# Performance work log

Measured on AMD Instinct MI355X. Metric: run time of the kernel, lower is better.

## Reference

```python
import jax, jax.numpy as jnp
import numpy as np
import math

N_HEADS = 16

def _apply_rope(t, cos, sin):
    # t: [b, h, s, hd]; cos/sin: [s, hd//2] (interleaved pairs, llama2.c style)
    b, h, s, hd = t.shape
    tr = t.reshape(b, h, s, hd // 2, 2)
    x_r, x_i = tr[..., 0], tr[..., 1]
    c = cos[None, None, :, :]
    sn = sin[None, None, :, :]
    o_r = x_r * c - x_i * sn
    o_i = x_r * sn + x_i * c
    return jnp.stack([o_r, o_i], axis=-1).reshape(b, h, s, hd)

def setup_inputs() -> dict:
    key = jax.random.key(0)
    ks = jax.random.split(key, 7)
    b, s, d = 4, 2048, 2048
    hd = d // N_HEADS
    x = jax.random.normal(ks[0], (b, s, d), dtype=jnp.float32)
    # RoPE tables: cos/sin of theta * pos, standard 10000 base
    inv_freq = 1.0 / (10000.0 ** (np.arange(0, hd, 2, dtype=np.float32) / hd))
    pos = np.arange(s, dtype=np.float32)
    ang = np.outer(pos, inv_freq)  # [s, hd/2]
    freq_cos = jnp.asarray(np.cos(ang), dtype=jnp.float32)
    freq_sin = jnp.asarray(np.sin(ang), dtype=jnp.float32)
    Wqkv = jax.random.normal(ks[1], (d, 3 * d), dtype=jnp.float32) * (1.0 / math.sqrt(d))
    bqkv = jnp.zeros((3 * d,), dtype=jnp.float32)
    Wout = jax.random.normal(ks[2], (d, d), dtype=jnp.float32) * (1.0 / math.sqrt(d))
    bout = jnp.zeros((d,), dtype=jnp.float32)
    return {"x": x, "freq_cos": freq_cos, "freq_sin": freq_sin,
            "Wqkv": Wqkv, "bqkv": bqkv, "Wout": Wout, "bout": bout}

def reference(x, freq_cos, freq_sin, Wqkv, bqkv, Wout, bout):
    b, s, d = x.shape
    hd = d // N_HEADS
    qkv = x @ Wqkv + bqkv                       # [b, s, 3d]
    q, k, v = jnp.split(qkv, 3, axis=-1)
    def to_heads(t):
        return t.reshape(b, s, N_HEADS, hd).transpose(0, 2, 1, 3)  # [b, h, s, hd]
    q, k, v = to_heads(q), to_heads(k), to_heads(v)
    q = _apply_rope(q, freq_cos, freq_sin)
    k = _apply_rope(k, freq_cos, freq_sin)
    att = jnp.einsum('bhqd,bhkd->bhqk', q, k) / math.sqrt(hd)
    mask = jnp.tril(jnp.ones((s, s), dtype=bool))
    att = jnp.where(mask[None, None, :, :], att, -jnp.inf)
    att = jax.nn.softmax(att, axis=-1)
    y = jnp.einsum('bhqk,bhkd->bhqd', att, v)
    y = y.transpose(0, 2, 1, 3).reshape(b, s, d)
    return y @ Wout + bout
```

## Files before the change

kernel.cpp:

```cpp
#include <hip/hip_runtime.h>

typedef __attribute__((ext_vector_type(4))) float f32x4;
typedef __attribute__((ext_vector_type(8))) short bf16x8;
typedef __attribute__((ext_vector_type(4))) unsigned int uint4v;
typedef __attribute__((ext_vector_type(4))) unsigned short ushort4v;
typedef unsigned short u16;
typedef unsigned int u32;

#define AS1(p) ((const __attribute__((address_space(1))) u32*)(p))
#define AS3(p) ((__attribute__((address_space(3))) u32*)(p))

__device__ __forceinline__ float bf2f(u16 v) {
    u32 u = ((u32)v) << 16;
    return __builtin_bit_cast(float, u);
}
__device__ __forceinline__ u16 f2bf(float f) {
    u32 u = __builtin_bit_cast(u32, f);
    u += 0x7fffu + ((u >> 16) & 1u);
    return (u16)(u >> 16);
}

__global__ __launch_bounds__(256) void k_cvt_bf16(const float* __restrict__ in,
                                                  u16* __restrict__ out, int n8) {
    int t = blockIdx.x * 256 + threadIdx.x;
    if (t >= n8) return;
    const f32x4* p = (const f32x4*)in + (size_t)t * 2;
    f32x4 a = p[0], b = p[1];
    uint4v o;
    o[0] = (u32)f2bf(a[0]) | ((u32)f2bf(a[1]) << 16);
    o[1] = (u32)f2bf(a[2]) | ((u32)f2bf(a[3]) << 16);
    o[2] = (u32)f2bf(b[0]) | ((u32)f2bf(b[1]) << 16);
    o[3] = (u32)f2bf(b[2]) | ((u32)f2bf(b[3]) << 16);
    *((uint4v*)(out + (size_t)t * 8)) = o;
}

__global__ __launch_bounds__(256) void k_transpose_bf16(const float* __restrict__ in,
                                                        u16* __restrict__ out,
                                                        int R, int C) {
    __shared__ float tile[32][33];
    const int bx = blockIdx.x * 32, by = blockIdx.y * 32;
    const int tx = threadIdx.x & 31, ty = threadIdx.x >> 5;
#pragma unroll
    for (int i = 0; i < 32; i += 8)
        tile[ty + i][tx] = in[(size_t)(by + ty + i) * C + bx + tx];
    __syncthreads();
#pragma unroll
    for (int i = 0; i < 32; i += 8)
        out[(size_t)(bx + ty + i) * R + by + tx] = f2bf(tile[tx][ty + i]);
}

template <int OUT_BF16>
__global__ __launch_bounds__(512, 2) void k_gemm256(const u16* __restrict__ A,
                                                    const u16* __restrict__ Bt,
                                                    const float* __restrict__ bias,
                                                    void* __restrict__ Cout,
                                                    int M, int N, int K) {
    __shared__ u16 lds[65536];
    const int tid = threadIdx.x;
    const int wid = tid >> 6, l = tid & 63;
    const int lr = l & 15, lg = l >> 4;
    const int wm = wid >> 2, wn = wid & 3;
    const size_t brow = (size_t)blockIdx.x * 256;
    const size_t bcol = (size_t)blockIdx.y * 256;
    const int KT = K >> 6;

    const u16* gA[4];
    const u16* gB[4];
#pragma unroll
    for (int r = 0; r < 4; ++r) {
        const int P = r * 8 + wid, g = P >> 1, kh = P & 1;
        const size_t off = (size_t)(g * 16 + lr) * K + kh * 32 + lg * 8;
        gA[r] = A + brow * K + off;
        gB[r] = Bt + bcol * K + off;
    }

    f32x4 acc[8][4];
#pragma unroll
    for (int m = 0; m < 8; ++m)
#pragma unroll
        for (int n = 0; n < 4; ++n) acc[m][n] = (f32x4){0.f, 0.f, 0.f, 0.f};

#define STAGE(t)                                                                        \
    do {                                                                                \
        const int b_ = (t) & 1;                                                         \
        const int k0_ = (t) << 6;                                                       \
        u16* dA_ = &lds[b_ * 16384];                                                    \
        u16* dB_ = &lds[32768 + b_ * 16384];                                            \
        __builtin_amdgcn_global_load_lds(AS1(gA[0] + k0_), AS3(dA_ + (0 * 8 + wid) * 512), 16, 0, 0); \
        __builtin_amdgcn_global_load_lds(AS1(gB[0] + k0_), AS3(dB_ + (0 * 8 + wid) * 512), 16, 0, 0); \
        __builtin_amdgcn_global_load_lds(AS1(gA[1] + k0_), AS3(dA_ + (1 * 8 + wid) * 512), 16, 0, 0); \
        __builtin_amdgcn_global_load_lds(AS1(gB[1] + k0_), AS3(dB_ + (1 * 8 + wid) * 512), 16, 0, 0); \
        __builtin_amdgcn_global_load_lds(AS1(gA[2] + k0_), AS3(dA_ + (2 * 8 + wid) * 512), 16, 0, 0); \
        __builtin_amdgcn_global_load_lds(AS1(gB[2] + k0_), AS3(dB_ + (2 * 8 + wid) * 512), 16, 0, 0); \
        __builtin_amdgcn_global_load_lds(AS1(gA[3] + k0_), AS3(dA_ + (3 * 8 + wid) * 512), 16, 0, 0); \
        __builtin_amdgcn_global_load_lds(AS1(gB[3] + k0_), AS3(dB_ + (3 * 8 + wid) * 512), 16, 0, 0); \
    } while (0)

    STAGE(0);
    asm volatile("s_waitcnt vmcnt(0)" ::: "memory");
    __builtin_amdgcn_s_barrier();
    __builtin_amdgcn_sched_barrier(0);

#pragma unroll 1
    for (int t = 0; t < KT; ++t) {
        if (t + 1 < KT) STAGE(t + 1);
        const u16* pa = &lds[(t & 1) * 16384 + wm * 8192 + l * 8];
        const u16* pb = &lds[32768 + (t & 1) * 16384 + wn * 4096 + l * 8];
#pragma unroll
        for (int ks = 0; ks < 2; ++ks) {
            bf16x8 af[8], bfr[4];
#pragma unroll
            for (int m = 0; m < 8; ++m) af[m] = *(const bf16x8*)(pa + (m * 2 + ks) * 512);
#pragma unroll
            for (int n = 0; n < 4; ++n) bfr[n] = *(const bf16x8*)(pb + (n * 2 + ks) * 512);
            __builtin_amdgcn_s_setprio(1);
#pragma unroll
            for (int m = 0; m < 8; ++m)
#pragma unroll
                for (int n = 0; n < 4; ++n)
                    acc[m][n] = __builtin_amdgcn_mfma_f32_16x16x32_bf16(af[m], bfr[n], acc[m][n], 0, 0, 0);
            __builtin_amdgcn_s_setprio(0);
        }
        __builtin_amdgcn_sched_barrier(0);
        asm volatile("s_waitcnt vmcnt(0)" ::: "memory");
        __builtin_amdgcn_s_barrier();
        __builtin_amdgcn_sched_barrier(0);
    }
#undef STAGE

#pragma unroll
    for (int m = 0; m < 8; ++m) {
        const size_t row0 = brow + wm * 128 + m * 16 + lg * 4;
#pragma unroll
        for (int n = 0; n < 4; ++n) {
            const size_t col = bcol + wn * 64 + n * 16 + lr;
            const float bv = bias[col];
#pragma unroll
            for (int r = 0; r < 4; ++r) {
                float v = acc[m][n][r] + bv;
                if (OUT_BF16)
                    ((u16*)Cout)[(row0 + r) * N + col] = f2bf(v);
                else
                    ((float*)Cout)[(row0 + r) * N + col] = v;
            }
        }
    }
}

__global__ __launch_bounds__(256) void k_rope(const u16* __restrict__ qkv,
                                              const float* __restrict__ fcos,
                                              const float* __restrict__ fsin,
                                              u16* __restrict__ qb, u16* __restrict__ kb) {
    const int t = blockIdx.x * 256 + threadIdx.x;
    const int e = t & 7, h = (t >> 3) & 15, r = (t >> 7) & 1, s = (t >> 8) & 2047, b = t >> 19;
    const u16* src = qkv + ((size_t)(b * 2048 + s)) * 6144 + r * 2048 + h * 128 + e * 16;
    uint4v p0 = *(const uint4v*)src;
    uint4v p1 = *(const uint4v*)(src + 8);
    const float* cp = fcos + s * 64 + e * 8;
    const float* sp = fsin + s * 64 + e * 8;
    f32x4 c0 = *(const f32x4*)cp, c1 = *(const f32x4*)(cp + 4);
    f32x4 s0 = *(const f32x4*)sp, s1 = *(const f32x4*)(sp + 4);
    float x[16];
#pragma unroll
    for (int i = 0; i < 4; ++i) {
        x[2 * i]     = bf2f((u16)(p0[i] & 0xffff));
        x[2 * i + 1] = bf2f((u16)(p0[i] >> 16));
        x[8 + 2 * i]     = bf2f((u16)(p1[i] & 0xffff));
        x[8 + 2 * i + 1] = bf2f((u16)(p1[i] >> 16));
    }
    float c[8]  = {c0[0], c0[1], c0[2], c0[3], c1[0], c1[1], c1[2], c1[3]};
    float sn[8] = {s0[0], s0[1], s0[2], s0[3], s1[0], s1[1], s1[2], s1[3]};
    u32 ow[8];
#pragma unroll
    for (int i = 0; i < 8; ++i) {
        float xr = x[2 * i], xi = x[2 * i + 1];
        float orr = xr * c[i] - xi * sn[i];
        float oii = xr * sn[i] + xi * c[i];
        ow[i] = (u32)f2bf(orr) | ((u32)f2bf(oii) << 16);
    }
    u16* dst = (r ? kb : qb) + ((size_t)((b * 16 + h) * 2048 + s)) * 128 + e * 16;
    uint4v q0 = {ow[0], ow[1], ow[2], ow[3]};
    uint4v q1 = {ow[4], ow[5], ow[6], ow[7]};
    *(uint4v*)dst = q0;
    *(uint4v*)(dst + 8) = q1;
}

struct VtRegs { uint4v v0, v1, v2, v3; };

__device__ __forceinline__ void attn_stage_k(const u16* kp, int kbase, u16* dstBase,
                                             int w, int lr, int lg) {
#pragma unroll
    for (int c = 0; c < 4; ++c) {
        const int row = w * 16 + c * 4 + lg;
        const int sslot = lr ^ (4 * (c & 1) + lg);
        const u16* gsrc = kp + (size_t)(kbase + row) * 128 + sslot * 8;
        __builtin_amdgcn_global_load_lds(AS1(gsrc), AS3(dstBase + (w * 16 + c * 4) * 128), 16, 0, 0);
    }
}

__device__ __forceinline__ VtRegs attn_load_v(const u16* vp, int kbase, int tid) {
    const int rg = tid >> 4, cg = tid & 15;
    const u16* gv = vp + (size_t)(kbase + rg * 4) * 6144 + cg * 8;
    VtRegs r;
    r.v0 = *(const uint4v*)gv;
    r.v1 = *(const uint4v*)(gv + 6144);
    r.v2 = *(const uint4v*)(gv + 2 * 6144);
    r.v3 = *(const uint4v*)(gv + 3 * 6144);
    return r;
}

__device__ __forceinline__ void attn_write_v(u16 (*Vt)[64], const VtRegs& r, int tid) {
    const int rg = tid >> 4, cg = tid & 15;
    const u16* u0 = (const u16*)&r.v0;
    const u16* u1 = (const u16*)&r.v1;
    const u16* u2 = (const u16*)&r.v2;
    const u16* u3 = (const u16*)&r.v3;
    const int sb = rg >> 1, hf = (rg & 1) * 4;
#pragma unroll
    for (int cc = 0; cc < 8; ++cc) {
        const int row = cg * 8 + cc;
        const int col = ((sb ^ ((cg ^ cc) & 7)) << 3) + hf;
        ushort4v pk = {u0[cc], u1[cc], u2[cc], u3[cc]};
        *(ushort4v*)&Vt[row][col] = pk;
    }
}

__device__ __forceinline__ void attn_qtile(int qt, const u16* qp, const u16* kp,
                                           const u16* vp, u16* yp,
                                           u16 (*Ks)[64][128], u16 (*Vt)[64],
                                           u16 (*Psw)[72],
                                           int w, int lr, int lg, int tid) {
    const int qw = qt * 128 + w * 32;
    const int l = tid & 63;

    bf16x8 qf[2][4];
#pragma unroll
    for (int i = 0; i < 2; ++i)
#pragma unroll
        for (int ks = 0; ks < 4; ++ks)
            qf[i][ks] = *(const bf16x8*)(qp + (size_t)(qw + i * 16 + lr) * 128 + ks * 32 + lg * 8);

    f32x4 acc[2][8];
#pragma unroll
    for (int i = 0; i < 2; ++i)
#pragma unroll
        for (int j = 0; j < 8; ++j) acc[i][j] = (f32x4){0.f, 0.f, 0.f, 0.f};
    float mrow[2] = {-1e30f, -1e30f}, lrow[2] = {0.f, 0.f};

    const float scale = 0.08838834764831845f;
    const int nkt = 2 * qt + 2;

    VtRegs vr = attn_load_v(vp, 0, tid);
    attn_stage_k(kp, 0, &Ks[0][0][0], w, lr, lg);
    attn_write_v(Vt, vr, tid);
    __syncthreads();

    int cur = 0;
    for (int kt = 0; kt < nkt; ++kt) {
        const int kbase = kt * 64;
        const bool pf = (kt + 1 < nkt);
        if (pf) {
            vr = attn_load_v(vp, kbase + 64, tid);
            attn_stage_k(kp, kbase + 64, &Ks[cur ^ 1][0][0], w, lr, lg);
        }

        if (kbase <= qw + 31) {
            f32x4 st[2][4];
#pragma unroll
            for (int i = 0; i < 2; ++i)
#pragma unroll
                for (int j = 0; j < 4; ++j) st[i][j] = (f32x4){0.f, 0.f, 0.f, 0.f};
#pragma unroll
            for (int nt = 0; nt < 4; ++nt) {
#pragma unroll
                for (int ks = 0; ks < 4; ++ks) {
                    const int slot = (ks * 4 + lg) ^ (lr & 7);
                    bf16x8 kf = *(const bf16x8*)&Ks[cur][nt * 16 + lr][slot * 8];
#pragma unroll
                    for (int mt = 0; mt < 2; ++mt)
                        st[mt][nt] = __builtin_amdgcn_mfma_f32_16x16x32_bf16(kf, qf[mt][ks], st[mt][nt], 0, 0, 0);
                }
            }
            const bool pm = (kbase + 63 > qw);
#pragma unroll
            for (int mt = 0; mt < 2; ++mt)
#pragma unroll
                for (int nt = 0; nt < 4; ++nt)
#pragma unroll
                    for (int r = 0; r < 4; ++r) {
                        float v = st[mt][nt][r] * scale;
                        if (pm) {
                            const int qi = qw + mt * 16 + lr;
                            const int ki = kbase + nt * 16 + lg * 4 + r;
                            if (ki > qi) v = -1e30f;
                        }
                        st[mt][nt][r] = v;
                    }
            float rm[2], fac[2];
#pragma unroll
            for (int mt = 0; mt < 2; ++mt) {
                float m0 = st[mt][0][0];
#pragma unroll
                for (int nt = 0; nt < 4; ++nt)
#pragma unroll
                    for (int r = 0; r < 4; ++r) m0 = fmaxf(m0, st[mt][nt][r]);
                m0 = fmaxf(m0, __shfl_xor(m0, 16));
                m0 = fmaxf(m0, __shfl_xor(m0, 32));
                rm[mt] = m0;
                const float mn = fmaxf(mrow[mt], m0);
                fac[mt] = __expf(mrow[mt] - mn);
                mrow[mt] = mn;
                lrow[mt] *= fac[mt];
            }
            float facr[2][4];
#pragma unroll
            for (int mt = 0; mt < 2; ++mt)
#pragma unroll
                for (int r = 0; r < 4; ++r)
                    facr[mt][r] = __shfl(fac[mt], (l & 48) | (lg * 4 + r));
#pragma unroll
            for (int mt = 0; mt < 2; ++mt)
#pragma unroll
                for (int nt = 0; nt < 8; ++nt)
#pragma unroll
                    for (int r = 0; r < 4; ++r) acc[mt][nt][r] *= facr[mt][r];
#pragma unroll
            for (int mt = 0; mt < 2; ++mt) {
                float rs = 0.f;
#pragma unroll
                for (int nt = 0; nt < 4; ++nt)
#pragma unroll
                    for (int r = 0; r < 4; ++r) {
                        const float p = __expf(st[mt][nt][r] - mrow[mt]);
                        st[mt][nt][r] = p;
                        rs += p;
                    }
                rs += __shfl_xor(rs, 16);
                rs += __shfl_xor(rs, 32);
                lrow[mt] += rs;
            }
#pragma unroll
            for (int mt = 0; mt < 2; ++mt)
#pragma unroll
                for (int nt = 0; nt < 4; ++nt) {
                    const u32 p01 = (u32)f2bf(st[mt][nt][0]) | ((u32)f2bf(st[mt][nt][1]) << 16);
                    const u32 p23 = (u32)f2bf(st[mt][nt][2]) | ((u32)f2bf(st[mt][nt][3]) << 16);
                    u16* dst = &Psw[mt * 16 + lr][nt * 16 + lg * 4];
                    *(u32*)dst = p01;
                    *(u32*)(dst + 2) = p23;
                }
#pragma unroll
            for (int k2 = 0; k2 < 2; ++k2) {
                bf16x8 pa[2];
                pa[0] = *(const bf16x8*)&Psw[lr][k2 * 32 + lg * 8];
                pa[1] = *(const bf16x8*)&Psw[16 + lr][k2 * 32 + lg * 8];
#pragma unroll
                for (int nt = 0; nt < 8; ++nt) {
                    const int f = ((nt * 2 + (lr >> 3)) ^ lr) & 7;
                    const int slot = (k2 * 4 + lg) ^ f;
                    bf16x8 vb = *(const bf16x8*)&Vt[nt * 16 + lr][slot * 8];
#pragma unroll
                    for (int mt = 0; mt < 2; ++mt)
                        acc[mt][nt] = __builtin_amdgcn_mfma_f32_16x16x32_bf16(pa[mt], vb, acc[mt][nt], 0, 0, 0);
                }
            }
        }

        __builtin_amdgcn_s_barrier();
        __builtin_amdgcn_sched_barrier(0);
        if (pf) {
            asm volatile("s_waitcnt vmcnt(4)" ::: "memory");
            attn_write_v(Vt, vr, tid);
            asm volatile("s_waitcnt vmcnt(0) lgkmcnt(0)" ::: "memory");
        } else {
            asm volatile("s_waitcnt vmcnt(0) lgkmcnt(0)" ::: "memory");
        }
        __builtin_amdgcn_s_barrier();
        __builtin_amdgcn_sched_barrier(0);
        cur ^= 1;
    }

#pragma unroll
    for (int mt = 0; mt < 2; ++mt)
#pragma unroll
        for (int r = 0; r < 4; ++r) {
            const float lsum = __shfl(lrow[mt], (l & 48) | (lg * 4 + r));
            const float inv = 1.f / lsum;
            const size_t row = qw + mt * 16 + lg * 4 + r;
#pragma unroll
            for (int nt = 0; nt < 8; ++nt)
                yp[row * 2048 + nt * 16 + lr] = f2bf(acc[mt][nt][r] * inv);
        }
}

__global__ __launch_bounds__(256, 2) void k_attn(const u16* __restrict__ qb,
                                                 const u16* __restrict__ kb,
                                                 const u16* __restrict__ qkv,
                                                 u16* __restrict__ yb) {
    __shared__ u16 Ks[2][64][128];
    __shared__ u16 Vt[128][64];
    __shared__ u16 Ps[4][32][72];

    const int gid = blockIdx.x;
    const int x = gid >> 6;
    const int g = gid & 63;
    const int h = g & 15, b = g >> 4;
    const int tid = threadIdx.x;
    const int w = tid >> 6, l = tid & 63;
    const int lr = l & 15, lg = l >> 4;

    const u16* qp = qb + (size_t)((b * 16 + h) * 2048) * 128;
    const u16* kp = kb + (size_t)((b * 16 + h) * 2048) * 128;
    const u16* vp = qkv + (size_t)(b * 2048) * 6144 + 4096 + h * 128;
    u16* yp = yb + (size_t)(b * 2048) * 2048 + h * 128;

    attn_qtile(x,      qp, kp, vp, yp, Ks, Vt, Ps[w], w, lr, lg, tid);
    attn_qtile(15 - x, qp, kp, vp, yp, Ks, Vt, Ps[w], w, lr, lg, tid);
}

extern "C" void kernel_launch(void* const* d_in, const int* in_sizes, int n_in,
                              void* d_out, int out_size, void* d_ws, size_t ws_size,
                              hipStream_t stream) {
    const float* x    = (const float*)d_in[0];
    const float* fcos = (const float*)d_in[1];
    const float* fsin = (const float*)d_in[2];
    const float* Wqkv = (const float*)d_in[3];
    const float* bqkv = (const float*)d_in[4];
    const float* Wout = (const float*)d_in[5];
    const float* bout = (const float*)d_in[6];
    float* out = (float*)d_out;

    if (ws_size < 234881024u) return;

    char* ws = (char*)d_ws;
    u16* x_bf  = (u16*)(ws);
    u16* wqkvT = (u16*)(ws + 33554432);
    u16* woutT = (u16*)(ws + 58720256);
    u16* qkv   = (u16*)(ws + 67108864);
    u16* qb    = (u16*)(ws + 167772160);
    u16* kb    = (u16*)(ws + 201326592);
    u16* yb    = x_bf;

    k_cvt_bf16<<<8192, 256, 0, stream>>>(x, x_bf, 2097152);
    k_transpose_bf16<<<dim3(192, 64), 256, 0, stream>>>(Wqkv, wqkvT, 2048, 6144);
    k_transpose_bf16<<<dim3(64, 64), 256, 0, stream>>>(Wout, woutT, 2048, 2048);
    k_gemm256<1><<<dim3(32, 24), 512, 0, stream>>>(x_bf, wqkvT, bqkv, qkv, 8192, 6144, 2048);
    k_rope<<<8192, 256, 0, stream>>>(qkv, fcos, fsin, qb, kb);
    k_attn<<<512, 256, 0, stream>>>(qb, kb, qkv, yb);
    k_gemm256<0><<<dim3(32, 8), 512, 0, stream>>>(yb, woutT, bout, out, 8192, 2048, 2048);
}
```

Before: 559.0 us.

## Restructure GEMM main loop into phased quadrant schedule with finer-grained prefetch

Rewrites the 256x256 GEMM K-loop into an unrolled two-tile iteration split into four quadrant phases per tile. Each phase loads a sub-fragment from LDS, issues one slice of the global-to-LDS prefetch for the next tile, and runs its MFMAs between barriers, with partial vmcnt waits in place of full drains. The aim is to interleave memory traffic with compute more evenly and cut register pressure per phase. Launch bounds drop to one block per SM, giving more registers in exchange for less occupancy, and the many extra barriers add synchronisation cost.

New measurement: 519.1 us. 1.08x faster.

```diff
diff --git a/kernel.cpp b/kernel.cpp
--- a/kernel.cpp
+++ b/kernel.cpp
@@ -50,7 +50,7 @@
 }
 
 template <int OUT_BF16>
-__global__ __launch_bounds__(512, 2) void k_gemm256(const u16* __restrict__ A,
+__global__ __launch_bounds__(512, 1) void k_gemm256(const u16* __restrict__ A,
                                                     const u16* __restrict__ Bt,
                                                     const float* __restrict__ bias,
                                                     void* __restrict__ Cout,
@@ -63,16 +63,28 @@
     const size_t brow = (size_t)blockIdx.x * 256;
     const size_t bcol = (size_t)blockIdx.y * 256;
     const int KT = K >> 6;
-
-    const u16* gA[4];
-    const u16* gB[4];
-#pragma unroll
-    for (int r = 0; r < 4; ++r) {
-        const int P = r * 8 + wid, g = P >> 1, kh = P & 1;
-        const size_t off = (size_t)(g * 16 + lr) * K + kh * 32 + lg * 8;
-        gA[r] = A + brow * K + off;
-        gB[r] = Bt + bcol * K + off;
-    }
+    const int NJ = KT >> 1;
+
+    const u16* gArow = A + brow * K;
+    const u16* gBrow = Bt + bcol * K;
+    const size_t laneoff = (size_t)lr * K + lg * 8;
+    const int gA1 = (wid & 3) | ((wid & 4) << 1);
+    const int gA2 = gA1 + 4;
+    const int gB1 = (wid & 1) | ((wid & 6) << 1);
+    const int gB2 = gB1 + 2;
+
+    auto STG = [&](const u16* gbase, int opBase, int g, int tt) {
+        u16* dst = &lds[opBase + ((tt) & 1) * 16384 + g * 1024];
+        const u16* src = gbase + (size_t)g * 16 * K + (size_t)tt * 64 + laneoff;
+        __builtin_amdgcn_global_load_lds(AS1(src), AS3(dst), 16, 0, 0);
+        __builtin_amdgcn_global_load_lds(AS1(src + 32), AS3(dst + 512), 16, 0, 0);
+    };
+    auto LDA_ = [&](int slot, int m, int ks) {
+        return *(const bf16x8*)&lds[slot * 16384 + ((wm * 8 + m) * 2 + ks) * 512 + l * 8];
+    };
+    auto LDB_ = [&](int slot, int n, int ks) {
+        return *(const bf16x8*)&lds[32768 + slot * 16384 + ((wn * 4 + n) * 2 + ks) * 512 + l * 8];
+    };
 
     f32x4 acc[8][4];
 #pragma unroll
@@ -80,53 +92,164 @@
 #pragma unroll
         for (int n = 0; n < 4; ++n) acc[m][n] = (f32x4){0.f, 0.f, 0.f, 0.f};
 
-#define STAGE(t)                                                                        \
-    do {                                                                                \
-        const int b_ = (t) & 1;                                                         \
-        const int k0_ = (t) << 6;                                                       \
-        u16* dA_ = &lds[b_ * 16384];                                                    \
-        u16* dB_ = &lds[32768 + b_ * 16384];                                            \
-        __builtin_amdgcn_global_load_lds(AS1(gA[0] + k0_), AS3(dA_ + (0 * 8 + wid) * 512), 16, 0, 0); \
-        __builtin_amdgcn_global_load_lds(AS1(gB[0] + k0_), AS3(dB_ + (0 * 8 + wid) * 512), 16, 0, 0); \
-        __builtin_amdgcn_global_load_lds(AS1(gA[1] + k0_), AS3(dA_ + (1 * 8 + wid) * 512), 16, 0, 0); \
-        __builtin_amdgcn_global_load_lds(AS1(gB[1] + k0_), AS3(dB_ + (1 * 8 + wid) * 512), 16, 0, 0); \
-        __builtin_amdgcn_global_load_lds(AS1(gA[2] + k0_), AS3(dA_ + (2 * 8 + wid) * 512), 16, 0, 0); \
-        __builtin_amdgcn_global_load_lds(AS1(gB[2] + k0_), AS3(dB_ + (2 * 8 + wid) * 512), 16, 0, 0); \
-        __builtin_amdgcn_global_load_lds(AS1(gA[3] + k0_), AS3(dA_ + (3 * 8 + wid) * 512), 16, 0, 0); \
-        __builtin_amdgcn_global_load_lds(AS1(gB[3] + k0_), AS3(dB_ + (3 * 8 + wid) * 512), 16, 0, 0); \
-    } while (0)
-
-    STAGE(0);
-    asm volatile("s_waitcnt vmcnt(0)" ::: "memory");
+    STG(gArow, 0, gA1, 0); STG(gBrow, 32768, gB1, 0);
+    STG(gArow, 0, gA2, 0); STG(gBrow, 32768, gB2, 0);
+    STG(gArow, 0, gA1, 1); STG(gBrow, 32768, gB1, 1);
+    STG(gArow, 0, gA2, 1);
+    asm volatile("s_waitcnt vmcnt(6)" ::: "memory");
     __builtin_amdgcn_s_barrier();
-    __builtin_amdgcn_sched_barrier(0);
+
+#define OPEN_PHASE()                                              \
+    __builtin_amdgcn_s_barrier();                                 \
+    asm volatile("s_waitcnt lgkmcnt(0)" ::: "memory");            \
+    __builtin_amdgcn_sched_barrier(0);                            \
+    __builtin_amdgcn_s_setprio(1);
+#define CLOSE_PHASE()                                             \
+    __builtin_amdgcn_s_setprio(0);                                \
+    __builtin_amdgcn_sched_barrier(0);                            \
+    __builtin_amdgcn_s_barrier();
 
 #pragma unroll 1
-    for (int t = 0; t < KT; ++t) {
-        if (t + 1 < KT) STAGE(t + 1);
-        const u16* pa = &lds[(t & 1) * 16384 + wm * 8192 + l * 8];
-        const u16* pb = &lds[32768 + (t & 1) * 16384 + wn * 4096 + l * 8];
-#pragma unroll
-        for (int ks = 0; ks < 2; ++ks) {
-            bf16x8 af[8], bfr[4];
-#pragma unroll
-            for (int m = 0; m < 8; ++m) af[m] = *(const bf16x8*)(pa + (m * 2 + ks) * 512);
-#pragma unroll
-            for (int n = 0; n < 4; ++n) bfr[n] = *(const bf16x8*)(pb + (n * 2 + ks) * 512);
-            __builtin_amdgcn_s_setprio(1);
-#pragma unroll
-            for (int m = 0; m < 8; ++m)
-#pragma unroll
-                for (int n = 0; n < 4; ++n)
-                    acc[m][n] = __builtin_amdgcn_mfma_f32_16x16x32_bf16(af[m], bfr[n], acc[m][n], 0, 0, 0);
-            __builtin_amdgcn_s_setprio(0);
-        }
-        __builtin_amdgcn_sched_barrier(0);
-        asm volatile("s_waitcnt vmcnt(0)" ::: "memory");
+    for (int j = 0; j < NJ; ++j) {
+        const int t0 = 2 * j, t1 = 2 * j + 1;
+        const bool pf = (j + 1 < NJ);
+        bf16x8 a[4][2], b0[2][2], b1[2][2];
+
+#pragma unroll
+        for (int m = 0; m < 4; ++m)
+#pragma unroll
+            for (int ks = 0; ks < 2; ++ks) a[m][ks] = LDA_(0, m, ks);
+#pragma unroll
+        for (int n = 0; n < 2; ++n)
+#pragma unroll
+            for (int ks = 0; ks < 2; ++ks) b0[n][ks] = LDB_(0, n, ks);
+        STG(gBrow, 32768, gB2, t1);
+        OPEN_PHASE();
+#pragma unroll
+        for (int m = 0; m < 4; ++m)
+#pragma unroll
+            for (int n = 0; n < 2; ++n)
+#pragma unroll
+                for (int ks = 0; ks < 2; ++ks)
+                    acc[m][n] = __builtin_amdgcn_mfma_f32_16x16x32_bf16(a[m][ks], b0[n][ks], acc[m][n], 0, 0, 0);
+        CLOSE_PHASE();
+
+#pragma unroll
+        for (int n = 0; n < 2; ++n)
+#pragma unroll
+            for (int ks = 0; ks < 2; ++ks) b1[n][ks] = LDB_(0, n + 2, ks);
+        if (pf) STG(gArow, 0, gA1, t0 + 2);
+        OPEN_PHASE();
+#pragma unroll
+        for (int m = 0; m < 4; ++m)
+#pragma unroll
+            for (int n = 0; n < 2; ++n)
+#pragma unroll
+                for (int ks = 0; ks < 2; ++ks)
+                    acc[m][n + 2] = __builtin_amdgcn_mfma_f32_16x16x32_bf16(a[m][ks], b1[n][ks], acc[m][n + 2], 0, 0, 0);
+        CLOSE_PHASE();
+
+#pragma unroll
+        for (int m = 0; m < 4; ++m)
+#pragma unroll
+            for (int ks = 0; ks < 2; ++ks) a[m][ks] = LDA_(0, m + 4, ks);
+        if (pf) STG(gBrow, 32768, gB1, t0 + 2);
+        OPEN_PHASE();
+#pragma unroll
+        for (int m = 0; m < 4; ++m)
+#pragma unroll
+            for (int n = 0; n < 2; ++n)
+#pragma unroll
+                for (int ks = 0; ks < 2; ++ks)
+                    acc[m + 4][n] = __builtin_amdgcn_mfma_f32_16x16x32_bf16(a[m][ks], b0[n][ks], acc[m + 4][n], 0, 0, 0);
+        CLOSE_PHASE();
+
+        if (pf) STG(gArow, 0, gA2, t0 + 2);
         __builtin_amdgcn_s_barrier();
         __builtin_amdgcn_sched_barrier(0);
-    }
-#undef STAGE
+        __builtin_amdgcn_s_setprio(1);
+#pragma unroll
+        for (int m = 0; m < 4; ++m)
+#pragma unroll
+            for (int n = 0; n < 2; ++n)
+#pragma unroll
+                for (int ks = 0; ks < 2; ++ks)
+                    acc[m + 4][n + 2] = __builtin_amdgcn_mfma_f32_16x16x32_bf16(a[m][ks], b1[n][ks], acc[m + 4][n + 2], 0, 0, 0);
+        __builtin_amdgcn_s_setprio(0);
+        __builtin_amdgcn_sched_barrier(0);
+        if (pf) asm volatile("s_waitcnt vmcnt(6)" ::: "memory");
+        else    asm volatile("s_waitcnt vmcnt(0)" ::: "memory");
+        __builtin_amdgcn_s_barrier();
+
+#pragma unroll
+        for (int m = 0; m < 4; ++m)
+#pragma unroll
+            for (int ks = 0; ks < 2; ++ks) a[m][ks] = LDA_(1, m, ks);
+#pragma unroll
+        for (int n = 0; n < 2; ++n)
+#pragma unroll
+            for (int ks = 0; ks < 2; ++ks) b0[n][ks] = LDB_(1, n, ks);
+        if (pf) STG(gBrow, 32768, gB2, t0 + 2);
+        OPEN_PHASE();
+#pragma unroll
+        for (int m = 0; m < 4; ++m)
+#pragma unroll
+            for (int n = 0; n < 2; ++n)
+#pragma unroll
+                for (int ks = 0; ks < 2; ++ks)
+                    acc[m][n] = __builtin_amdgcn_mfma_f32_16x16x32_bf16(a[m][ks], b0[n][ks], acc[m][n], 0, 0, 0);
+        CLOSE_PHASE();
+
+#pragma unroll
+        for (int n = 0; n < 2; ++n)
+#pragma unroll
+            for (int ks = 0; ks < 2; ++ks) b1[n][ks] = LDB_(1, n + 2, ks);
+        if (pf) STG(gArow, 0, gA1, t1 + 2);
+        OPEN_PHASE();
+#pragma unroll
+        for (int m = 0; m < 4; ++m)
+#pragma unroll
+            for (int n = 0; n < 2; ++n)
+#pragma unroll
+                for (int ks = 0; ks < 2; ++ks)
+                    acc[m][n + 2] = __builtin_amdgcn_mfma_f32_16x16x32_bf16(a[m][ks], b1[n][ks], acc[m][n + 2], 0, 0, 0);
+        CLOSE_PHASE();
+
+#pragma unroll
+        for (int m = 0; m < 4; ++m)
+#pragma unroll
+            for (int ks = 0; ks < 2; ++ks) a[m][ks] = LDA_(1, m + 4, ks);
+        if (pf) STG(gBrow, 32768, gB1, t1 + 2);
+        OPEN_PHASE();
+#pragma unroll
+        for (int m = 0; m < 4; ++m)
+#pragma unroll
+            for (int n = 0; n < 2; ++n)
+#pragma unroll
+                for (int ks = 0; ks < 2; ++ks)
+                    acc[m + 4][n] = __builtin_amdgcn_mfma_f32_16x16x32_bf16(a[m][ks], b0[n][ks], acc[m + 4][n], 0, 0, 0);
+        CLOSE_PHASE();
+
+        if (pf) STG(gArow, 0, gA2, t1 + 2);
+        __builtin_amdgcn_s_barrier();
+        __builtin_amdgcn_sched_barrier(0);
+        __builtin_amdgcn_s_setprio(1);
+#pragma unroll
+        for (int m = 0; m < 4; ++m)
+#pragma unroll
+            for (int n = 0; n < 2; ++n)
+#pragma unroll
+                for (int ks = 0; ks < 2; ++ks)
+                    acc[m + 4][n + 2] = __builtin_amdgcn_mfma_f32_16x16x32_bf16(a[m][ks], b1[n][ks], acc[m + 4][n + 2], 0, 0, 0);
+        __builtin_amdgcn_s_setprio(0);
+        __builtin_amdgcn_sched_barrier(0);
+        if (pf) {
+            asm volatile("s_waitcnt vmcnt(6)" ::: "memory");
+            __builtin_amdgcn_s_barrier();
+        }
+    }
+#undef OPEN_PHASE
+#undef CLOSE_PHASE
 
 #pragma unroll
     for (int m = 0; m < 8; ++m) {
```

## Rewrite GEMM main loop as 8-phase ping-pong schedule with interleaved prefetch

Applied to the files above, without the earlier changes.

Restructures the 256x256 bf16 GEMM main loop into a two-k-tile unrolled, eight-phase schedule. Each phase interleaves LDS fragment reads, partial global->LDS prefetches and a quarter of the MFMA block, with fine-grained lgkmcnt/vmcnt waits and barriers in place of one full wait per tile. The aim is to overlap memory traffic with matrix math and avoid stalls at tile boundaries. Launch bounds drop to one block per CU to give more registers for the doubled fragment buffers, at the cost of occupancy and added barrier overhead.

Result: slower. 1.250 ms (+123.7%).

```diff
diff --git a/kernel.cpp b/kernel.cpp
--- a/kernel.cpp
+++ b/kernel.cpp
@@ -50,7 +50,7 @@
 }
 
 template <int OUT_BF16>
-__global__ __launch_bounds__(512, 2) void k_gemm256(const u16* __restrict__ A,
+__global__ __launch_bounds__(512, 1) void k_gemm256(const u16* __restrict__ A,
                                                     const u16* __restrict__ Bt,
                                                     const float* __restrict__ bias,
                                                     void* __restrict__ Cout,
@@ -63,16 +63,28 @@
     const size_t brow = (size_t)blockIdx.x * 256;
     const size_t bcol = (size_t)blockIdx.y * 256;
     const int KT = K >> 6;
-
-    const u16* gA[4];
-    const u16* gB[4];
-#pragma unroll
-    for (int r = 0; r < 4; ++r) {
-        const int P = r * 8 + wid, g = P >> 1, kh = P & 1;
-        const size_t off = (size_t)(g * 16 + lr) * K + kh * 32 + lg * 8;
-        gA[r] = A + brow * K + off;
-        gB[r] = Bt + bcol * K + off;
-    }
+    const int NJ = KT >> 1;
+
+    const u16* gArow = A + brow * K;
+    const u16* gBrow = Bt + bcol * K;
+    const size_t laneoff = (size_t)lr * K + lg * 8;
+    const int gA1 = (wid & 3) | ((wid & 4) << 1);
+    const int gA2 = gA1 + 4;
+    const int gB1 = (wid & 1) | ((wid & 6) << 1);
+    const int gB2 = gB1 + 2;
+
+    auto STG = [&](const u16* gbase, int opBase, int g, int tt) {
+        u16* dst = &lds[opBase + (tt & 1) * 16384 + g * 1024];
+        const u16* src = gbase + (size_t)g * 16 * K + (size_t)tt * 64 + laneoff;
+        __builtin_amdgcn_global_load_lds(AS1(src), AS3(dst), 16, 0, 0);
+        __builtin_amdgcn_global_load_lds(AS1(src + 32), AS3(dst + 512), 16, 0, 0);
+    };
+    auto LDA_ = [&](int slot, int m, int ks) {
+        return *(const bf16x8*)&lds[slot * 16384 + ((wm * 8 + m) * 2 + ks) * 512 + l * 8];
+    };
+    auto LDB_ = [&](int slot, int n, int ks) {
+        return *(const bf16x8*)&lds[32768 + slot * 16384 + ((wn * 4 + n) * 2 + ks) * 512 + l * 8];
+    };
 
     f32x4 acc[8][4];
 #pragma unroll
@@ -80,53 +92,115 @@
 #pragma unroll
         for (int n = 0; n < 4; ++n) acc[m][n] = (f32x4){0.f, 0.f, 0.f, 0.f};
 
-#define STAGE(t)                                                                        \
-    do {                                                                                \
-        const int b_ = (t) & 1;                                                         \
-        const int k0_ = (t) << 6;                                                       \
-        u16* dA_ = &lds[b_ * 16384];                                                    \
-        u16* dB_ = &lds[32768 + b_ * 16384];                                            \
-        __builtin_amdgcn_global_load_lds(AS1(gA[0] + k0_), AS3(dA_ + (0 * 8 + wid) * 512), 16, 0, 0); \
-        __builtin_amdgcn_global_load_lds(AS1(gB[0] + k0_), AS3(dB_ + (0 * 8 + wid) * 512), 16, 0, 0); \
-        __builtin_amdgcn_global_load_lds(AS1(gA[1] + k0_), AS3(dA_ + (1 * 8 + wid) * 512), 16, 0, 0); \
-        __builtin_amdgcn_global_load_lds(AS1(gB[1] + k0_), AS3(dB_ + (1 * 8 + wid) * 512), 16, 0, 0); \
-        __builtin_amdgcn_global_load_lds(AS1(gA[2] + k0_), AS3(dA_ + (2 * 8 + wid) * 512), 16, 0, 0); \
-        __builtin_amdgcn_global_load_lds(AS1(gB[2] + k0_), AS3(dB_ + (2 * 8 + wid) * 512), 16, 0, 0); \
-        __builtin_amdgcn_global_load_lds(AS1(gA[3] + k0_), AS3(dA_ + (3 * 8 + wid) * 512), 16, 0, 0); \
-        __builtin_amdgcn_global_load_lds(AS1(gB[3] + k0_), AS3(dB_ + (3 * 8 + wid) * 512), 16, 0, 0); \
-    } while (0)
-
-    STAGE(0);
-    asm volatile("s_waitcnt vmcnt(0)" ::: "memory");
+    bf16x8 aEl[4][2], aEh[4][2], bEl[2][2], bEh[2][2];
+    bf16x8 aOl[4][2], aOh[4][2], bOl[2][2], bOh[2][2];
+
+#define RD_AEL() { _Pragma("unroll") for (int m = 0; m < 4; ++m) _Pragma("unroll") for (int ks = 0; ks < 2; ++ks) aEl[m][ks] = LDA_(0, m, ks); }
+#define RD_AEH() { _Pragma("unroll") for (int m = 0; m < 4; ++m) _Pragma("unroll") for (int ks = 0; ks < 2; ++ks) aEh[m][ks] = LDA_(0, m + 4, ks); }
+#define RD_BEL() { _Pragma("unroll") for (int n = 0; n < 2; ++n) _Pragma("unroll") for (int ks = 0; ks < 2; ++ks) bEl[n][ks] = LDB_(0, n, ks); }
+#define RD_BEH() { _Pragma("unroll") for (int n = 0; n < 2; ++n) _Pragma("unroll") for (int ks = 0; ks < 2; ++ks) bEh[n][ks] = LDB_(0, n + 2, ks); }
+#define RD_AOL() { _Pragma("unroll") for (int m = 0; m < 4; ++m) _Pragma("unroll") for (int ks = 0; ks < 2; ++ks) aOl[m][ks] = LDA_(1, m, ks); }
+#define RD_AOH() { _Pragma("unroll") for (int m = 0; m < 4; ++m) _Pragma("unroll") for (int ks = 0; ks < 2; ++ks) aOh[m][ks] = LDA_(1, m + 4, ks); }
+#define RD_BOL() { _Pragma("unroll") for (int n = 0; n < 2; ++n) _Pragma("unroll") for (int ks = 0; ks < 2; ++ks) bOl[n][ks] = LDB_(1, n, ks); }
+#define RD_BOH() { _Pragma("unroll") for (int n = 0; n < 2; ++n) _Pragma("unroll") for (int ks = 0; ks < 2; ++ks) bOh[n][ks] = LDB_(1, n + 2, ks); }
+
+#define MM(AR, BR, MO, NO)                                                              \
+    { _Pragma("unroll") for (int m = 0; m < 4; ++m)                                     \
+      _Pragma("unroll") for (int n = 0; n < 2; ++n)                                     \
+      _Pragma("unroll") for (int ks = 0; ks < 2; ++ks)                                  \
+          acc[m + MO][n + NO] = __builtin_amdgcn_mfma_f32_16x16x32_bf16(                \
+              AR[m][ks], BR[n][ks], acc[m + MO][n + NO], 0, 0, 0); }
+
+#define SBZ() __builtin_amdgcn_sched_barrier(0)
+#define OPEN(nlg)                                                  \
+    SBZ(); __builtin_amdgcn_s_barrier();                           \
+    asm volatile("s_waitcnt lgkmcnt(" #nlg ")" ::: "memory");      \
+    SBZ(); __builtin_amdgcn_s_setprio(1);
+#define CLOSE()                                                    \
+    __builtin_amdgcn_s_setprio(0); SBZ();                          \
     __builtin_amdgcn_s_barrier();
-    __builtin_amdgcn_sched_barrier(0);
+
+    STG(gArow, 0, gA1, 0); STG(gBrow, 32768, gB1, 0);
+    STG(gArow, 0, gA2, 0); STG(gBrow, 32768, gB2, 0);
+    STG(gArow, 0, gA1, 1); STG(gBrow, 32768, gB1, 1);
+    STG(gArow, 0, gA2, 1);
+    asm volatile("s_waitcnt vmcnt(6)" ::: "memory");
+    __builtin_amdgcn_s_barrier();
+    RD_AEL(); RD_BEL();
 
 #pragma unroll 1
-    for (int t = 0; t < KT; ++t) {
-        if (t + 1 < KT) STAGE(t + 1);
-        const u16* pa = &lds[(t & 1) * 16384 + wm * 8192 + l * 8];
-        const u16* pb = &lds[32768 + (t & 1) * 16384 + wn * 4096 + l * 8];
-#pragma unroll
-        for (int ks = 0; ks < 2; ++ks) {
-            bf16x8 af[8], bfr[4];
-#pragma unroll
-            for (int m = 0; m < 8; ++m) af[m] = *(const bf16x8*)(pa + (m * 2 + ks) * 512);
-#pragma unroll
-            for (int n = 0; n < 4; ++n) bfr[n] = *(const bf16x8*)(pb + (n * 2 + ks) * 512);
-            __builtin_amdgcn_s_setprio(1);
-#pragma unroll
-            for (int m = 0; m < 8; ++m)
-#pragma unroll
-                for (int n = 0; n < 4; ++n)
-                    acc[m][n] = __builtin_amdgcn_mfma_f32_16x16x32_bf16(af[m], bfr[n], acc[m][n], 0, 0, 0);
-            __builtin_amdgcn_s_setprio(0);
+    for (int j = 0; j < NJ; ++j) {
+        const int t0 = 2 * j, t1 = 2 * j + 1;
+        const bool pf = (j + 1 < NJ);
+
+        RD_AEH();
+        STG(gBrow, 32768, gB2, t1);
+        OPEN(8);
+        MM(aEl, bEl, 0, 0);
+        CLOSE();
+
+        RD_BEH();
+        if (pf) STG(gArow, 0, gA1, t0 + 2);
+        OPEN(4);
+        MM(aEh, bEl, 4, 0);
+        CLOSE();
+
+        if (pf) STG(gBrow, 32768, gB1, t0 + 2);
+        OPEN(0);
+        MM(aEh, bEh, 4, 2);
+        __builtin_amdgcn_s_setprio(0); SBZ();
+        if (pf) asm volatile("s_waitcnt vmcnt(4)" ::: "memory");
+        else    asm volatile("s_waitcnt vmcnt(0)" ::: "memory");
+        __builtin_amdgcn_s_barrier();
+
+        RD_AOL(); RD_BOL();
+        if (pf) STG(gArow, 0, gA2, t0 + 2);
+        OPEN(12);
+        MM(aEl, bEh, 0, 2);
+        CLOSE();
+
+        RD_AOH();
+        if (pf) STG(gBrow, 32768, gB2, t0 + 2);
+        OPEN(8);
+        MM(aOl, bOl, 0, 0);
+        CLOSE();
+
+        RD_BOH();
+        if (pf) STG(gArow, 0, gA1, t1 + 2);
+        OPEN(4);
+        MM(aOh, bOl, 4, 0);
+        CLOSE();
+
+        if (pf) STG(gBrow, 32768, gB1, t1 + 2);
+        OPEN(0);
+        MM(aOh, bOh, 4, 2);
+        __builtin_amdgcn_s_setprio(0); SBZ();
+        if (pf) asm volatile("s_waitcnt vmcnt(4)" ::: "memory");
+        else    asm volatile("s_waitcnt vmcnt(0)" ::: "memory");
+        __builtin_amdgcn_s_barrier();
+
+        if (pf) {
+            RD_AEL(); RD_BEL();
+            STG(gArow, 0, gA2, t1 + 2);
+            OPEN(12);
+        } else {
+            OPEN(0);
         }
-        __builtin_amdgcn_sched_barrier(0);
-        asm volatile("s_waitcnt vmcnt(0)" ::: "memory");
-        __builtin_amdgcn_s_barrier();
-        __builtin_amdgcn_sched_barrier(0);
-    }
-#undef STAGE
+        MM(aOl, bOh, 0, 2);
+        CLOSE();
+    }
+#undef RD_AEL
+#undef RD_AEH
+#undef RD_BEL
+#undef RD_BEH
+#undef RD_AOL
+#undef RD_AOH
+#undef RD_BOL
+#undef RD_BOH
+#undef MM
+#undef SBZ
+#undef OPEN
+#undef CLOSE
 
 #pragma unroll
     for (int m = 0; m < 8; ++m) {
```

## Shrink GEMM tiles to 128x256 with K=32 steps and XCD-aware block mapping

Applied to the files above, without the earlier changes.

Replaces the 256x256, K=64 GEMM tile with a 128x256 tile stepping through K in chunks of 32. This cuts LDS use from 128KB to 48KB and the accumulators from 8x4 to 4x4, so launch bounds can allow 4 blocks per CU. Blocks are remapped from a 1D grid so that each XCD owns a contiguous range of column tiles, aiming for better L2 reuse of B. The trade-off is less data reuse per tile, twice as many barriers per K, and more global traffic for A/B overall.

After: 623.1 us (median of 2 runs). 1.11x slower.

```diff
diff --git a/kernel.cpp b/kernel.cpp
--- a/kernel.cpp
+++ b/kernel.cpp
@@ -50,50 +50,41 @@
 }
 
 template <int OUT_BF16>
-__global__ __launch_bounds__(512, 2) void k_gemm256(const u16* __restrict__ A,
+__global__ __launch_bounds__(512, 4) void k_gemm128(const u16* __restrict__ A,
                                                     const u16* __restrict__ Bt,
                                                     const float* __restrict__ bias,
                                                     void* __restrict__ Cout,
                                                     int M, int N, int K) {
-    __shared__ u16 lds[65536];
+    __shared__ u16 lds[24576];
     const int tid = threadIdx.x;
     const int wid = tid >> 6, l = tid & 63;
     const int lr = l & 15, lg = l >> 4;
     const int wm = wid >> 2, wn = wid & 3;
-    const size_t brow = (size_t)blockIdx.x * 256;
-    const size_t bcol = (size_t)blockIdx.y * 256;
-    const int KT = K >> 6;
-
-    const u16* gA[4];
-    const u16* gB[4];
-#pragma unroll
-    for (int r = 0; r < 4; ++r) {
-        const int P = r * 8 + wid, g = P >> 1, kh = P & 1;
-        const size_t off = (size_t)(g * 16 + lr) * K + kh * 32 + lg * 8;
-        gA[r] = A + brow * K + off;
-        gB[r] = Bt + bcol * K + off;
-    }
-
-    f32x4 acc[8][4];
-#pragma unroll
-    for (int m = 0; m < 8; ++m)
+    const int nbrow = M >> 7;
+    const int nbcol = N >> 8;
+    const int xcd = blockIdx.x & 7, id2 = blockIdx.x >> 3;
+    const int colPerXcd = nbcol >> 3;
+    const size_t brow = (size_t)(id2 % nbrow) * 128;
+    const size_t bcol = (size_t)(xcd * colPerXcd + id2 / nbrow) * 256;
+    const int KT = K >> 5;
+
+    const u16* gA  = A  + (brow + (size_t)wid * 16 + lr) * K + lg * 8;
+    const u16* gB0 = Bt + (bcol + (size_t)wid * 16 + lr) * K + lg * 8;
+    const u16* gB1 = Bt + (bcol + (size_t)(wid + 8) * 16 + lr) * K + lg * 8;
+
+    f32x4 acc[4][4];
+#pragma unroll
+    for (int m = 0; m < 4; ++m)
 #pragma unroll
         for (int n = 0; n < 4; ++n) acc[m][n] = (f32x4){0.f, 0.f, 0.f, 0.f};
 
-#define STAGE(t)                                                                        \
-    do {                                                                                \
-        const int b_ = (t) & 1;                                                         \
-        const int k0_ = (t) << 6;                                                       \
-        u16* dA_ = &lds[b_ * 16384];                                                    \
-        u16* dB_ = &lds[32768 + b_ * 16384];                                            \
-        __builtin_amdgcn_global_load_lds(AS1(gA[0] + k0_), AS3(dA_ + (0 * 8 + wid) * 512), 16, 0, 0); \
-        __builtin_amdgcn_global_load_lds(AS1(gB[0] + k0_), AS3(dB_ + (0 * 8 + wid) * 512), 16, 0, 0); \
-        __builtin_amdgcn_global_load_lds(AS1(gA[1] + k0_), AS3(dA_ + (1 * 8 + wid) * 512), 16, 0, 0); \
-        __builtin_amdgcn_global_load_lds(AS1(gB[1] + k0_), AS3(dB_ + (1 * 8 + wid) * 512), 16, 0, 0); \
-        __builtin_amdgcn_global_load_lds(AS1(gA[2] + k0_), AS3(dA_ + (2 * 8 + wid) * 512), 16, 0, 0); \
-        __builtin_amdgcn_global_load_lds(AS1(gB[2] + k0_), AS3(dB_ + (2 * 8 + wid) * 512), 16, 0, 0); \
-        __builtin_amdgcn_global_load_lds(AS1(gA[3] + k0_), AS3(dA_ + (3 * 8 + wid) * 512), 16, 0, 0); \
-        __builtin_amdgcn_global_load_lds(AS1(gB[3] + k0_), AS3(dB_ + (3 * 8 + wid) * 512), 16, 0, 0); \
+#define STAGE(t)                                                                                     \
+    do {                                                                                             \
+        const int b_ = (t) & 1;                                                                      \
+        const int k0_ = (t) << 5;                                                                    \
+        __builtin_amdgcn_global_load_lds(AS1(gA + k0_),  AS3(&lds[b_ * 4096 + wid * 512]), 16, 0, 0);\
+        __builtin_amdgcn_global_load_lds(AS1(gB0 + k0_), AS3(&lds[8192 + b_ * 8192 + wid * 512]), 16, 0, 0); \
+        __builtin_amdgcn_global_load_lds(AS1(gB1 + k0_), AS3(&lds[8192 + b_ * 8192 + (wid + 8) * 512]), 16, 0, 0); \
     } while (0)
 
     STAGE(0);
@@ -104,33 +95,30 @@
 #pragma unroll 1
     for (int t = 0; t < KT; ++t) {
         if (t + 1 < KT) STAGE(t + 1);
-        const u16* pa = &lds[(t & 1) * 16384 + wm * 8192 + l * 8];
-        const u16* pb = &lds[32768 + (t & 1) * 16384 + wn * 4096 + l * 8];
-#pragma unroll
-        for (int ks = 0; ks < 2; ++ks) {
-            bf16x8 af[8], bfr[4];
-#pragma unroll
-            for (int m = 0; m < 8; ++m) af[m] = *(const bf16x8*)(pa + (m * 2 + ks) * 512);
-#pragma unroll
-            for (int n = 0; n < 4; ++n) bfr[n] = *(const bf16x8*)(pb + (n * 2 + ks) * 512);
-            __builtin_amdgcn_s_setprio(1);
-#pragma unroll
-            for (int m = 0; m < 8; ++m)
-#pragma unroll
-                for (int n = 0; n < 4; ++n)
-                    acc[m][n] = __builtin_amdgcn_mfma_f32_16x16x32_bf16(af[m], bfr[n], acc[m][n], 0, 0, 0);
-            __builtin_amdgcn_s_setprio(0);
-        }
+        const u16* pa = &lds[(t & 1) * 4096 + (wm * 4) * 512 + l * 8];
+        const u16* pb = &lds[8192 + (t & 1) * 8192 + (wn * 4) * 512 + l * 8];
+        bf16x8 af[4], bfr[4];
+#pragma unroll
+        for (int m = 0; m < 4; ++m) af[m] = *(const bf16x8*)(pa + m * 512);
+#pragma unroll
+        for (int n = 0; n < 4; ++n) bfr[n] = *(const bf16x8*)(pb + n * 512);
+        __builtin_amdgcn_s_setprio(1);
+#pragma unroll
+        for (int m = 0; m < 4; ++m)
+#pragma unroll
+            for (int n = 0; n < 4; ++n)
+                acc[m][n] = __builtin_amdgcn_mfma_f32_16x16x32_bf16(af[m], bfr[n], acc[m][n], 0, 0, 0);
+        __builtin_amdgcn_s_setprio(0);
         __builtin_amdgcn_sched_barrier(0);
-        asm volatile("s_waitcnt vmcnt(0)" ::: "memory");
+        if (t + 1 < KT) asm volatile("s_waitcnt vmcnt(0)" ::: "memory");
         __builtin_amdgcn_s_barrier();
         __builtin_amdgcn_sched_barrier(0);
     }
 #undef STAGE
 
 #pragma unroll
-    for (int m = 0; m < 8; ++m) {
-        const size_t row0 = brow + wm * 128 + m * 16 + lg * 4;
+    for (int m = 0; m < 4; ++m) {
+        const size_t row0 = brow + wm * 64 + m * 16 + lg * 4;
 #pragma unroll
         for (int n = 0; n < 4; ++n) {
             const size_t col = bcol + wn * 64 + n * 16 + lr;
@@ -444,8 +432,8 @@
     k_cvt_bf16<<<8192, 256, 0, stream>>>(x, x_bf, 2097152);
     k_transpose_bf16<<<dim3(192, 64), 256, 0, stream>>>(Wqkv, wqkvT, 2048, 6144);
     k_transpose_bf16<<<dim3(64, 64), 256, 0, stream>>>(Wout, woutT, 2048, 2048);
-    k_gemm256<1><<<dim3(32, 24), 512, 0, stream>>>(x_bf, wqkvT, bqkv, qkv, 8192, 6144, 2048);
+    k_gemm128<1><<<1536, 512, 0, stream>>>(x_bf, wqkvT, bqkv, qkv, 8192, 6144, 2048);
     k_rope<<<8192, 256, 0, stream>>>(qkv, fcos, fsin, qb, kb);
     k_attn<<<512, 256, 0, stream>>>(qb, kb, qkv, yb);
-    k_gemm256<0><<<dim3(32, 8), 512, 0, stream>>>(yb, woutT, bout, out, 8192, 2048, 2048);
-}
+    k_gemm128<0><<<512, 512, 0, stream>>>(yb, woutT, bout, out, 8192, 2048, 2048);
+}
```
